# Kernel tuning notes

Measured on AMD Instinct MI355X. Metric: run time of the kernel, lower is better.

The kernel has to match this reference:

```python
import jax, jax.numpy as jnp
import numpy as np

E = 200_000   # edges (messages)
T = 2_000_000 # triplets
N = 20_000    # atoms/nodes
H = 128       # hidden_channels
INT = 64      # int_emb_size
BAS = 8       # basis_emb_size
OUT_EMB = 256 # out_emb_channels
NRAD = 6
SBF_DIM = 7 * 6  # num_spherical * num_radial = 42
NB = 4        # num_blocks
OUTC = 1      # num_targets


def setup_inputs() -> dict:
    key = jax.random.key(0)
    ks = iter(jax.random.split(key, 64))

    def w(shape):
        # glorot-ish scaled weights, stored as [in, out] for x @ W
        return jax.random.normal(next(ks), shape, jnp.float32) / np.sqrt(shape[-2])

    return dict(
        x=jax.random.normal(next(ks), (E, H), jnp.float32),
        rbf=jax.random.normal(next(ks), (E, NRAD), jnp.float32),
        sbf=jax.random.normal(next(ks), (T, SBF_DIM), jnp.float32),
        # interaction block params, stacked over NB blocks
        W_rbf1=w((NB, NRAD, BAS)), W_rbf2=w((NB, BAS, H)),
        W_sbf1=w((NB, SBF_DIM, BAS)), W_sbf2=w((NB, BAS, INT)),
        W_kj=w((NB, H, H)), b_kj=jnp.zeros((NB, H), jnp.float32),
        W_ji=w((NB, H, H)), b_ji=jnp.zeros((NB, H), jnp.float32),
        W_down=w((NB, H, INT)), W_up=w((NB, INT, H)),
        Wb=w((NB, 2, H, H)), bb=jnp.zeros((NB, 2, H), jnp.float32),   # num_before_skip=1 -> 2 linears
        Wa=w((NB, 4, H, H)), ba=jnp.zeros((NB, 4, H), jnp.float32),   # num_after_skip=2 -> 4 linears
        W_lin=w((NB, H, H)), b_lin=jnp.zeros((NB, H), jnp.float32),
        # output block params, stacked over NB+1 blocks
        Wo_rbf=w((NB + 1, NRAD, H)),
        Wo_up=w((NB + 1, H, OUT_EMB)), bo_up=jnp.zeros((NB + 1, OUT_EMB), jnp.float32),
        Wo_lins=w((NB + 1, 3, OUT_EMB, OUT_EMB)), bo_lins=jnp.zeros((NB + 1, 3, OUT_EMB), jnp.float32),
        Wo_out=w((NB + 1, OUT_EMB, OUTC)),
        idx_kj=jax.random.randint(next(ks), (T,), 0, E, jnp.int32),
        idx_ji=jax.random.randint(next(ks), (T,), 0, E, jnp.int32),
        idx_i=jax.random.randint(next(ks), (E,), 0, N, jnp.int32),
        num_nodes=N,
    )


def _interaction(b, x, rbf, sbf, idx_kj, idx_ji, p):
    act = jax.nn.silu
    x_ji = act(x @ p['W_ji'][b] + p['b_ji'][b])
    x_kj = act(x @ p['W_kj'][b] + p['b_kj'][b])
    rbf_t = (rbf @ p['W_rbf1'][b]) @ p['W_rbf2'][b]          # [E,H]
    x_kj = act((x_kj * rbf_t) @ p['W_down'][b])              # [E,INT]
    sbf_t = (sbf @ p['W_sbf1'][b]) @ p['W_sbf2'][b]          # [T,INT]
    m = x_kj[idx_kj] * sbf_t                                  # triplet gather [T,INT]
    agg = jax.ops.segment_sum(m, idx_ji, num_segments=x.shape[0])  # scatter-add [E,INT]
    x_kj = act(agg @ p['W_up'][b])                            # [E,H]
    h = x_ji + x_kj
    # residual layers before skip (1 layer = 2 linears)
    h = h + act(act(h @ p['Wb'][b, 0] + p['bb'][b, 0]) @ p['Wb'][b, 1] + p['bb'][b, 1])
    h = act(h @ p['W_lin'][b] + p['b_lin'][b]) + x
    # residual layers after skip (2 layers = 4 linears)
    for l in range(2):
        h = h + act(act(h @ p['Wa'][b, 2 * l] + p['ba'][b, 2 * l]) @ p['Wa'][b, 2 * l + 1] + p['ba'][b, 2 * l + 1])
    return h


def _output(b, x, rbf, idx_i, num_nodes, p):
    act = jax.nn.silu
    t = (rbf @ p['Wo_rbf'][b]) * x                            # [E,H]
    t = jax.ops.segment_sum(t, idx_i, num_segments=num_nodes) # [N,H]
    t = t @ p['Wo_up'][b] + p['bo_up'][b]
    for l in range(3):
        t = act(t @ p['Wo_lins'][b, l] + p['bo_lins'][b, l])
    return t @ p['Wo_out'][b]                                 # [N,OUTC]


def reference(x, rbf, sbf, W_rbf1, W_rbf2, W_sbf1, W_sbf2, W_kj, b_kj, W_ji, b_ji,
              W_down, W_up, Wb, bb, Wa, ba, W_lin, b_lin,
              Wo_rbf, Wo_up, bo_up, Wo_lins, bo_lins, Wo_out,
              idx_kj, idx_ji, idx_i, num_nodes):
    p = dict(W_rbf1=W_rbf1, W_rbf2=W_rbf2, W_sbf1=W_sbf1, W_sbf2=W_sbf2,
             W_kj=W_kj, b_kj=b_kj, W_ji=W_ji, b_ji=b_ji, W_down=W_down, W_up=W_up,
             Wb=Wb, bb=bb, Wa=Wa, ba=ba, W_lin=W_lin, b_lin=b_lin,
             Wo_rbf=Wo_rbf, Wo_up=Wo_up, bo_up=bo_up,
             Wo_lins=Wo_lins, bo_lins=bo_lins, Wo_out=Wo_out)
    P = _output(0, x, rbf, idx_i, num_nodes, p)
    for b in range(NB):  # fixed small layer loop
        x = _interaction(b, x, rbf, sbf, idx_kj, idx_ji, p)
        P = P + _output(b + 1, x, rbf, idx_i, num_nodes, p)
    return P
```

## Files before the change

kernel.cpp:

```cpp
#include <hip/hip_runtime.h>
#include <hip/hip_bf16.h>

#define E_EDGES 200000
#define T_TRIP  2000000
#define N_NODES 20000
#define H_DIM   128
#define INT_DIM 64
#define BAS     8
#define OUT_EMB 256
#define NRAD    6
#define SBF_D   42
#define NB      4

typedef __attribute__((ext_vector_type(8))) __bf16 bf16x8;
typedef __attribute__((ext_vector_type(4))) float f32x4;
typedef unsigned short u16;

__device__ __forceinline__ float silu_f(float v) { return v / (1.0f + __expf(-v)); }

__device__ __forceinline__ u16 f2bf(float f) {
    unsigned int u = __float_as_uint(f);
    u += 0x7FFF + ((u >> 16) & 1);
    return (u16)(u >> 16);
}
__device__ __forceinline__ float bf2f(u16 h) {
    return __uint_as_float(((unsigned int)h) << 16);
}

__device__ __forceinline__ void st_split4(char* H, char* L, int row, int col0, int stride,
                                          const float v[4]) {
    ushort4 hh, ll;
    u16 h0 = f2bf(v[0]); ll.x = f2bf(v[0] - bf2f(h0)); hh.x = h0;
    u16 h1 = f2bf(v[1]); ll.y = f2bf(v[1] - bf2f(h1)); hh.y = h1;
    u16 h2 = f2bf(v[2]); ll.z = f2bf(v[2] - bf2f(h2)); hh.z = h2;
    u16 h3 = f2bf(v[3]); ll.w = f2bf(v[3] - bf2f(h3)); hh.w = h3;
    int off = (row * stride + col0 * 2) ^ ((row & 7) << 4);
    *reinterpret_cast<ushort4*>(H + off) = hh;
    *reinterpret_cast<ushort4*>(L + off) = ll;
}
__device__ __forceinline__ void ld_split4(const char* H, const char* L, int row, int col0,
                                          int stride, float v[4]) {
    int off = (row * stride + col0 * 2) ^ ((row & 7) << 4);
    ushort4 hh = *reinterpret_cast<const ushort4*>(H + off);
    ushort4 ll = *reinterpret_cast<const ushort4*>(L + off);
    v[0] = bf2f(hh.x) + bf2f(ll.x);
    v[1] = bf2f(hh.y) + bf2f(ll.y);
    v[2] = bf2f(hh.z) + bf2f(ll.z);
    v[3] = bf2f(hh.w) + bf2f(ll.w);
}
__device__ __forceinline__ void st_bf4(char* T, int row, int col0, int stride,
                                       const float v[4]) {
    ushort4 hh;
    hh.x = f2bf(v[0]); hh.y = f2bf(v[1]); hh.z = f2bf(v[2]); hh.w = f2bf(v[3]);
    int off = (row * stride + col0 * 2) ^ ((row & 7) << 4);
    *reinterpret_cast<ushort4*>(T + off) = hh;
}

struct BF8x4 { bf16x8 h[4]; bf16x8 l[4]; };

__device__ __forceinline__ BF8x4 loadB128f(const u16* __restrict__ Bh, const u16* __restrict__ Bl,
                                           int k0, int wn, int l15, int khalf)
{
    BF8x4 f;
    #pragma unroll
    for (int n = 0; n < 4; ++n) {
        size_t bo = (size_t)(wn * 64 + n * 16 + l15) * 128 + k0 + khalf;
        f.h[n] = *reinterpret_cast<const bf16x8*>(Bh + bo);
        f.l[n] = *reinterpret_cast<const bf16x8*>(Bl + bo);
    }
    return f;
}
__device__ __forceinline__ BF8x4 loadB64f(const u16* __restrict__ Bh, const u16* __restrict__ Bl,
                                          int k0, int wn, int l15, int khalf)
{
    BF8x4 f;
    #pragma unroll
    for (int n = 0; n < 4; ++n) {
        size_t bo = (size_t)(wn * 64 + n * 16 + l15) * 64 + k0 + khalf;
        f.h[n] = *reinterpret_cast<const bf16x8*>(Bh + bo);
        f.l[n] = *reinterpret_cast<const bf16x8*>(Bl + bo);
    }
    return f;
}
__device__ __forceinline__ BF8x4 loadB256f(const u16* __restrict__ Bh, const u16* __restrict__ Bl,
                                           int k0, int wn, int l15, int khalf)
{
    BF8x4 f;
    #pragma unroll
    for (int n = 0; n < 4; ++n) {
        size_t bo = (size_t)(wn * 64 + n * 16 + l15) * 256 + k0 + khalf;
        f.h[n] = *reinterpret_cast<const bf16x8*>(Bh + bo);
        f.l[n] = *reinterpret_cast<const bf16x8*>(Bl + bo);
    }
    return f;
}

__device__ __forceinline__ void mfma_cluster(
    const char* AH, const char* AL, int k0, int wm, int l15, int khalf,
    const BF8x4& b, f32x4 acc[2][4])
{
    __builtin_amdgcn_s_setprio(1);
    #pragma unroll
    for (int m = 0; m < 2; ++m) {
        int row = wm * 32 + m * 16 + l15;
        int off = (row * 256 + (k0 + khalf) * 2) ^ ((row & 7) << 4);
        bf16x8 ah = *reinterpret_cast<const bf16x8*>(AH + off);
        bf16x8 al = *reinterpret_cast<const bf16x8*>(AL + off);
        #pragma unroll
        for (int n = 0; n < 4; ++n) {
            acc[m][n] = __builtin_amdgcn_mfma_f32_16x16x32_bf16(b.h[n], ah, acc[m][n], 0, 0, 0);
            acc[m][n] = __builtin_amdgcn_mfma_f32_16x16x32_bf16(b.h[n], al, acc[m][n], 0, 0, 0);
            acc[m][n] = __builtin_amdgcn_mfma_f32_16x16x32_bf16(b.l[n], ah, acc[m][n], 0, 0, 0);
        }
    }
    __builtin_amdgcn_s_setprio(0);
}
__device__ __forceinline__ void mfma_cluster_T(
    const char* T, int k0, int wm, int l15, int khalf,
    const BF8x4& b, f32x4 acc[2][4])
{
    __builtin_amdgcn_s_setprio(1);
    #pragma unroll
    for (int m = 0; m < 2; ++m) {
        int row = wm * 32 + m * 16 + l15;
        int off = (row * 256 + (k0 + khalf) * 2) ^ ((row & 7) << 4);
        bf16x8 a = *reinterpret_cast<const bf16x8*>(T + off);
        #pragma unroll
        for (int n = 0; n < 4; ++n) {
            acc[m][n] = __builtin_amdgcn_mfma_f32_16x16x32_bf16(b.h[n], a, acc[m][n], 0, 0, 0);
            acc[m][n] = __builtin_amdgcn_mfma_f32_16x16x32_bf16(b.l[n], a, acc[m][n], 0, 0, 0);
        }
    }
    __builtin_amdgcn_s_setprio(0);
}
__device__ __forceinline__ void mfma_cluster64_T(
    const char* T, int k0, int wm, int l15, int khalf,
    const BF8x4& b, f32x4 acc[2][4])
{
    __builtin_amdgcn_s_setprio(1);
    #pragma unroll
    for (int m = 0; m < 2; ++m) {
        int row = wm * 32 + m * 16 + l15;
        int off = (row * 128 + (k0 + khalf) * 2) ^ ((row & 7) << 4);
        bf16x8 a = *reinterpret_cast<const bf16x8*>(T + off);
        #pragma unroll
        for (int n = 0; n < 4; ++n) {
            acc[m][n] = __builtin_amdgcn_mfma_f32_16x16x32_bf16(b.h[n], a, acc[m][n], 0, 0, 0);
            acc[m][n] = __builtin_amdgcn_mfma_f32_16x16x32_bf16(b.l[n], a, acc[m][n], 0, 0, 0);
        }
    }
    __builtin_amdgcn_s_setprio(0);
}
__device__ __forceinline__ void mfma_cluster512(
    const char* AH, const char* AL, int k0, int l15, int khalf,
    const BF8x4& b, f32x4 acc[2][4])
{
    __builtin_amdgcn_s_setprio(1);
    #pragma unroll
    for (int m = 0; m < 2; ++m) {
        int row = m * 16 + l15;
        int off = (row * 512 + (k0 + khalf) * 2) ^ ((row & 7) << 4);
        bf16x8 ah = *reinterpret_cast<const bf16x8*>(AH + off);
        bf16x8 al = *reinterpret_cast<const bf16x8*>(AL + off);
        #pragma unroll
        for (int n = 0; n < 4; ++n) {
            acc[m][n] = __builtin_amdgcn_mfma_f32_16x16x32_bf16(b.h[n], ah, acc[m][n], 0, 0, 0);
            acc[m][n] = __builtin_amdgcn_mfma_f32_16x16x32_bf16(b.h[n], al, acc[m][n], 0, 0, 0);
            acc[m][n] = __builtin_amdgcn_mfma_f32_16x16x32_bf16(b.l[n], ah, acc[m][n], 0, 0, 0);
        }
    }
    __builtin_amdgcn_s_setprio(0);
}
__device__ __forceinline__ void mfma_cluster512_T(
    const char* T, int k0, int l15, int khalf,
    const BF8x4& b, f32x4 acc[2][4])
{
    __builtin_amdgcn_s_setprio(1);
    #pragma unroll
    for (int m = 0; m < 2; ++m) {
        int row = m * 16 + l15;
        int off = (row * 512 + (k0 + khalf) * 2) ^ ((row & 7) << 4);
        bf16x8 a = *reinterpret_cast<const bf16x8*>(T + off);
        #pragma unroll
        for (int n = 0; n < 4; ++n) {
            acc[m][n] = __builtin_amdgcn_mfma_f32_16x16x32_bf16(b.h[n], a, acc[m][n], 0, 0, 0);
            acc[m][n] = __builtin_amdgcn_mfma_f32_16x16x32_bf16(b.l[n], a, acc[m][n], 0, 0, 0);
        }
    }
    __builtin_amdgcn_s_setprio(0);
}

__device__ __forceinline__ void mm128_pipe(
    const char* AH, const char* AL,
    const u16* __restrict__ Bh, const u16* __restrict__ Bl, BF8x4& pre,
    const u16* __restrict__ nBh, const u16* __restrict__ nBl,
    int wm, int wn, int l15, int khalf, f32x4 acc[2][4])
{
    BF8x4 c0 = pre;
    BF8x4 c1 = loadB128f(Bh, Bl, 32, wn, l15, khalf);
    mfma_cluster(AH, AL, 0, wm, l15, khalf, c0, acc);
    BF8x4 c2 = loadB128f(Bh, Bl, 64, wn, l15, khalf);
    mfma_cluster(AH, AL, 32, wm, l15, khalf, c1, acc);
    BF8x4 c3 = loadB128f(Bh, Bl, 96, wn, l15, khalf);
    mfma_cluster(AH, AL, 64, wm, l15, khalf, c2, acc);
    if (nBh) pre = loadB128f(nBh, nBl, 0, wn, l15, khalf);
    mfma_cluster(AH, AL, 96, wm, l15, khalf, c3, acc);
}
__device__ __forceinline__ void mm128_pipe_T(
    const char* T,
    const u16* __restrict__ Bh, const u16* __restrict__ Bl, BF8x4& pre,
    const u16* __restrict__ nBh, const u16* __restrict__ nBl,
    int wm, int wn, int l15, int khalf, f32x4 acc[2][4])
{
    BF8x4 c0 = pre;
    BF8x4 c1 = loadB128f(Bh, Bl, 32, wn, l15, khalf);
    mfma_cluster_T(T, 0, wm, l15, khalf, c0, acc);
    BF8x4 c2 = loadB128f(Bh, Bl, 64, wn, l15, khalf);
    mfma_cluster_T(T, 32, wm, l15, khalf, c1, acc);
    BF8x4 c3 = loadB128f(Bh, Bl, 96, wn, l15, khalf);
    mfma_cluster_T(T, 64, wm, l15, khalf, c2, acc);
    if (nBh) pre = loadB128f(nBh, nBl, 0, wn, l15, khalf);
    mfma_cluster_T(T, 96, wm, l15, khalf, c3, acc);
}
__device__ __forceinline__ void mm64_pipe_T(
    const char* T,
    const u16* __restrict__ Bh, const u16* __restrict__ Bl, BF8x4& pre,
    const u16* __restrict__ nBh, const u16* __restrict__ nBl,
    int wm, int wn, int l15, int khalf, f32x4 acc[2][4])
{
    BF8x4 c0 = pre;
    BF8x4 c1 = loadB64f(Bh, Bl, 32, wn, l15, khalf);
    mfma_cluster64_T(T, 0, wm, l15, khalf, c0, acc);
    if (nBh) pre = loadB128f(nBh, nBl, 0, wn, l15, khalf);
    mfma_cluster64_T(T, 32, wm, l15, khalf, c1, acc);
}

__global__ __launch_bounds__(256) void wprep(
    const float* __restrict__ src, u16* __restrict__ hi,
    u16* __restrict__ lo, int K, int N)
{
    int e = blockIdx.x * 256 + threadIdx.x;
    int total = K * N;
    if (e >= total) return;
    size_t base = (size_t)blockIdx.y * total;
    float a = src[base + e];
    int k = e / N, n = e - k * N;
    u16 h = f2bf(a);
    u16 l = f2bf(a - bf2f(h));
    hi[base + (size_t)n * K + k] = h;
    lo[base + (size_t)n * K + k] = l;
}

__global__ __launch_bounds__(256) void cvt_bf(
    const float* __restrict__ src, u16* __restrict__ dst, int n4)
{
    int i = blockIdx.x * 256 + threadIdx.x;
    if (i >= n4) return;
    float4 f = *reinterpret_cast<const float4*>(&src[(size_t)i * 4]);
    ushort4 o;
    o.x = f2bf(f.x); o.y = f2bf(f.y); o.z = f2bf(f.z); o.w = f2bf(f.w);
    *reinterpret_cast<ushort4*>(&dst[(size_t)i * 4]) = o;
}

__global__ __launch_bounds__(256, 2) void pre_fuse(
    const u16* __restrict__ X, const float* __restrict__ rbf,
    const float* __restrict__ W1,
    const u16* __restrict__ Wjih, const u16* __restrict__ Wjil, const float* __restrict__ bji,
    const u16* __restrict__ Wkjh, const u16* __restrict__ Wkjl, const float* __restrict__ bkj,
    const float* __restrict__ Wr2,
    const u16* __restrict__ Wdnh, const u16* __restrict__ Wdnl,
    u16* __restrict__ E1, u16* __restrict__ C1)
{
    __shared__ char smem[32768];
    char* XT = smem;
    char* IT = smem + 16384;

    const int tid  = threadIdx.x;
    const int lane = tid & 63;
    const int w    = tid >> 6;
    const int wm   = w >> 1, wn = w & 1;
    const int bm   = blockIdx.x * 64;
    const int l15  = lane & 15;
    const int khalf = (lane >> 4) * 8;
    const int r4   = (lane >> 4) * 4;

    BF8x4 pre = loadB128f(Wjih, Wjil, 0, wn, l15, khalf);

    {
        int r  = tid >> 2;
        int c0 = (tid & 3) * 32;
        const u16* p = &X[(size_t)(bm + r) * H_DIM + c0];
        const int swz = (r & 7) << 4;
        #pragma unroll
        for (int q = 0; q < 4; ++q) {
            uint4 v = *reinterpret_cast<const uint4*>(p + q * 8);
            int off = (r * 256 + c0 * 2 + q * 16) ^ swz;
            *reinterpret_cast<uint4*>(XT + off) = v;
        }
    }
    __syncthreads();

    {
        f32x4 acc[2][4] = {};
        mm128_pipe_T(XT, Wjih, Wjil, pre, Wkjh, Wkjl, wm, wn, l15, khalf, acc);
        #pragma unroll
        for (int n = 0; n < 4; ++n) {
            int col0 = wn * 64 + n * 16 + r4;
            float4 bv = *reinterpret_cast<const float4*>(&bji[col0]);
            #pragma unroll
            for (int m = 0; m < 2; ++m) {
                int row = wm * 32 + m * 16 + l15;
                ushort4 ob;
                ob.x = f2bf(silu_f(acc[m][n][0] + bv.x));
                ob.y = f2bf(silu_f(acc[m][n][1] + bv.y));
                ob.z = f2bf(silu_f(acc[m][n][2] + bv.z));
                ob.w = f2bf(silu_f(acc[m][n][3] + bv.w));
                *reinterpret_cast<ushort4*>(&E1[(size_t)(bm + row) * H_DIM + col0]) = ob;
            }
        }
    }
    {
        f32x4 acc[2][4] = {};
        mm128_pipe_T(XT, Wkjh, Wkjl, pre, nullptr, nullptr, wm, wn, l15, khalf, acc);
        float r8v[2][8];
        #pragma unroll
        for (int m = 0; m < 2; ++m) {
            int grow = bm + wm * 32 + m * 16 + l15;
            const float2* rp = reinterpret_cast<const float2*>(&rbf[(size_t)grow * NRAD]);
            float2 q0 = rp[0], q1 = rp[1], q2 = rp[2];
            float rv[NRAD] = {q0.x, q0.y, q1.x, q1.y, q2.x, q2.y};
            #pragma unroll
            for (int j = 0; j < 8; ++j) r8v[m][j] = 0.f;
            #pragma unroll
            for (int k = 0; k < NRAD; ++k)
                #pragma unroll
                for (int j = 0; j < 8; ++j)
                    r8v[m][j] = fmaf(rv[k], W1[k * BAS + j], r8v[m][j]);
        }
        #pragma unroll
        for (int n = 0; n < 4; ++n) {
            int col0 = wn * 64 + n * 16 + r4;
            float4 bvf = *reinterpret_cast<const float4*>(&bkj[col0]);
            float bv[4] = {bvf.x, bvf.y, bvf.z, bvf.w};
            float wrv[8][4];
            #pragma unroll
            for (int j = 0; j < 8; ++j) {
                float4 wf = *reinterpret_cast<const float4*>(&Wr2[j * H_DIM + col0]);
                wrv[j][0] = wf.x; wrv[j][1] = wf.y; wrv[j][2] = wf.z; wrv[j][3] = wf.w;
            }
            #pragma unroll
            for (int m = 0; m < 2; ++m) {
                int row = wm * 32 + m * 16 + l15;
                float v[4];
                #pragma unroll
                for (int r = 0; r < 4; ++r) {
                    float t = silu_f(acc[m][n][r] + bv[r]);
                    float g = 0.f;
                    #pragma unroll
                    for (int j = 0; j < 8; ++j)
                        g = fmaf(r8v[m][j], wrv[j][r], g);
                    v[r] = t * g;
                }
                st_bf4(IT, row, col0, 256, v);
            }
        }
    }
    __syncthreads();

    {
        f32x4 acc[2][2] = {};
        #pragma unroll
        for (int k0 = 0; k0 < 128; k0 += 32) {
            bf16x8 bh[2], bl[2];
            #pragma unroll
            for (int n = 0; n < 2; ++n) {
                size_t bo = (size_t)(wn * 32 + n * 16 + l15) * 128 + k0 + khalf;
                bh[n] = *reinterpret_cast<const bf16x8*>(Wdnh + bo);
                bl[n] = *reinterpret_cast<const bf16x8*>(Wdnl + bo);
            }
            __builtin_amdgcn_s_setprio(1);
            #pragma unroll
            for (int m = 0; m < 2; ++m) {
                int row = wm * 32 + m * 16 + l15;
                int off = (row * 256 + (k0 + khalf) * 2) ^ ((row & 7) << 4);
                bf16x8 a = *reinterpret_cast<const bf16x8*>(IT + off);
                #pragma unroll
                for (int n = 0; n < 2; ++n) {
                    acc[m][n] = __builtin_amdgcn_mfma_f32_16x16x32_bf16(bh[n], a, acc[m][n], 0, 0, 0);
                    acc[m][n] = __builtin_amdgcn_mfma_f32_16x16x32_bf16(bl[n], a, acc[m][n], 0, 0, 0);
                }
            }
            __builtin_amdgcn_s_setprio(0);
        }
        #pragma unroll
        for (int n = 0; n < 2; ++n) {
            int col0 = wn * 32 + n * 16 + r4;
            #pragma unroll
            for (int m = 0; m < 2; ++m) {
                int row = wm * 32 + m * 16 + l15;
                ushort4 ob;
                ob.x = f2bf(silu_f(acc[m][n][0]));
                ob.y = f2bf(silu_f(acc[m][n][1]));
                ob.z = f2bf(silu_f(acc[m][n][2]));
                ob.w = f2bf(silu_f(acc[m][n][3]));
                *reinterpret_cast<ushort4*>(&C1[(size_t)(bm + row) * INT_DIM + col0]) = ob;
            }
        }
    }
}

struct ChainP {
    const u16 *uph, *upl;
    const u16 *b0h, *b0l, *b1h, *b1l;
    const u16 *lnh, *lnl;
    const u16 *a0h, *a0l, *a1h, *a1l, *a2h, *a2l, *a3h, *a3l;
    const float *bb0, *bb1, *blin, *ba0, *ba1, *ba2, *ba3;
    int doPre;
    const float *rbfp, *preW1, *nbji, *nbkj, *nwr2;
    const u16 *njih, *njil, *nkjh, *nkjl, *ndnh, *ndnl;
    u16 *nE1, *nC1;
};
struct OutP {
    const float* TN;
    const u16 *Uh, *Ul; const float* bu;
    const u16 *L0h, *L0l; const float* b0;
    const u16 *L1h, *L1l; const float* b1;
    const u16 *L2h, *L2l; const float* b2;
    const float* Wo; float* P;
};

__device__ __forceinline__ void post_chain_body(
    char* smem, int bx,
    const u16* __restrict__ AGG, const u16* __restrict__ E1,
    const u16* __restrict__ X, const ChainP& p, u16* __restrict__ OUT)
{
    char* SH  = smem;
    char* SL  = smem + 16384;
    char* TMP = smem + 32768;
    char* GB  = TMP;

    const int tid  = threadIdx.x;
    const int lane = tid & 63;
    const int w    = tid >> 6;
    const int wm   = w >> 1, wn = w & 1;
    const int bm   = bx * 64;
    const int l15  = lane & 15;
    const int khalf = (lane >> 4) * 8;
    const int r4   = (lane >> 4) * 4;

    BF8x4 pre = loadB64f(p.uph, p.upl, 0, wn, l15, khalf);

    {
        int r  = tid >> 2;
        int c0 = (tid & 3) * 16;
        const ushort4* pg = reinterpret_cast<const ushort4*>(&AGG[(size_t)(bm + r) * INT_DIM + c0]);
        const int swz = (r & 7) << 4;
        #pragma unroll
        for (int q = 0; q < 4; ++q) {
            ushort4 v = pg[q];
            int off = (r * 128 + c0 * 2 + q * 8) ^ swz;
            *reinterpret_cast<ushort4*>(GB + off) = v;
        }
    }
    __syncthreads();

    f32x4 acc[2][4];
    #define ZACC { _Pragma("unroll") for (int m = 0; m < 2; ++m) \
                   _Pragma("unroll") for (int n = 0; n < 4; ++n) \
                       acc[m][n] = f32x4{0.f, 0.f, 0.f, 0.f}; }

    ZACC
    mm64_pipe_T(GB, p.uph, p.upl, pre, p.b0h, p.b0l, wm, wn, l15, khalf, acc);
    #pragma unroll
    for (int n = 0; n < 4; ++n) {
        int col0 = wn * 64 + n * 16 + r4;
        #pragma unroll
        for (int m = 0; m < 2; ++m) {
            int row = wm * 32 + m * 16 + l15;
            ushort4 e = *reinterpret_cast<const ushort4*>(&E1[(size_t)(bm + row) * H_DIM + col0]);
            float v[4];
            v[0] = bf2f(e.x) + silu_f(acc[m][n][0]);
            v[1] = bf2f(e.y) + silu_f(acc[m][n][1]);
            v[2] = bf2f(e.z) + silu_f(acc[m][n][2]);
            v[3] = bf2f(e.w) + silu_f(acc[m][n][3]);
            st_split4(SH, SL, row, col0, 256, v);
        }
    }
    __syncthreads();

    #define STAGE_PLAIN(WH, WL, BIAS, NWH, NWL)                                         \
    {                                                                                   \
        ZACC                                                                            \
        mm128_pipe(SH, SL, WH, WL, pre, NWH, NWL, wm, wn, l15, khalf, acc);             \
        _Pragma("unroll")                                                               \
        for (int n = 0; n < 4; ++n) {                                                   \
            int col0 = wn * 64 + n * 16 + r4;                                           \
            float4 bv = *reinterpret_cast<const float4*>(&BIAS[col0]);                  \
            _Pragma("unroll")                                                           \
            for (int m = 0; m < 2; ++m) {                                               \
                int row = wm * 32 + m * 16 + l15;                                       \
                float v[4];                                                             \
                v[0] = silu_f(acc[m][n][0] + bv.x);                                     \
                v[1] = silu_f(acc[m][n][1] + bv.y);                                     \
                v[2] = silu_f(acc[m][n][2] + bv.z);                                     \
                v[3] = silu_f(acc[m][n][3] + bv.w);                                     \
                st_bf4(TMP, row, col0, 256, v);                                         \
            }                                                                           \
        }                                                                               \
        __syncthreads();                                                                \
    }

    #define STAGE_RES(WH, WL, BIAS, NWH, NWL)                                           \
    {                                                                                   \
        ZACC                                                                            \
        mm128_pipe_T(TMP, WH, WL, pre, NWH, NWL, wm, wn, l15, khalf, acc);              \
        _Pragma("unroll")                                                               \
        for (int n = 0; n < 4; ++n) {                                                   \
            int col0 = wn * 64 + n * 16 + r4;                                           \
            float4 bv = *reinterpret_cast<const float4*>(&BIAS[col0]);                  \
            _Pragma("unroll")                                                           \
            for (int m = 0; m < 2; ++m) {                                               \
                int row = wm * 32 + m * 16 + l15;                                       \
                float v[4];                                                             \
                ld_split4(SH, SL, row, col0, 256, v);                                   \
                v[0] += silu_f(acc[m][n][0] + bv.x);                                    \
                v[1] += silu_f(acc[m][n][1] + bv.y);                                    \
                v[2] += silu_f(acc[m][n][2] + bv.z);                                    \
                v[3] += silu_f(acc[m][n][3] + bv.w);                                    \
                st_split4(SH, SL, row, col0, 256, v);                                   \
            }                                                                           \
        }                                                                               \
        __syncthreads();                                                                \
    }

    STAGE_PLAIN(p.b0h, p.b0l, p.bb0, p.b1h, p.b1l)
    STAGE_RES(p.b1h, p.b1l, p.bb1, p.lnh, p.lnl)

    {
        ZACC
        mm128_pipe(SH, SL, p.lnh, p.lnl, pre, p.a0h, p.a0l, wm, wn, l15, khalf, acc);
        __syncthreads();
        #pragma unroll
        for (int n = 0; n < 4; ++n) {
            int col0 = wn * 64 + n * 16 + r4;
            float4 bv = *reinterpret_cast<const float4*>(&p.blin[col0]);
            #pragma unroll
            for (int m = 0; m < 2; ++m) {
                int row = wm * 32 + m * 16 + l15;
                ushort4 xv = *reinterpret_cast<const ushort4*>(&X[(size_t)(bm + row) * H_DIM + col0]);
                float v[4];
                v[0] = silu_f(acc[m][n][0] + bv.x) + bf2f(xv.x);
                v[1] = silu_f(acc[m][n][1] + bv.y) + bf2f(xv.y);
                v[2] = silu_f(acc[m][n][2] + bv.z) + bf2f(xv.z);
                v[3] = silu_f(acc[m][n][3] + bv.w) + bf2f(xv.w);
                st_split4(SH, SL, row, col0, 256, v);
            }
        }
        __syncthreads();
    }

    STAGE_PLAIN(p.a0h, p.a0l, p.ba0, p.a1h, p.a1l)
    STAGE_RES(p.a1h, p.a1l, p.ba1, p.a2h, p.a2l)
    STAGE_PLAIN(p.a2h, p.a2l, p.ba2, p.a3h, p.a3l)

    {
        ZACC
        mm128_pipe_T(TMP, p.a3h, p.a3l, pre,
                     p.doPre ? p.njih : nullptr, p.doPre ? p.njil : nullptr,
                     wm, wn, l15, khalf, acc);
        #pragma unroll
        for (int n = 0; n < 4; ++n) {
            int col0 = wn * 64 + n * 16 + r4;
            float4 bv = *reinterpret_cast<const float4*>(&p.ba3[col0]);
            #pragma unroll
            for (int m = 0; m < 2; ++m) {
                int row = wm * 32 + m * 16 + l15;
                float v[4];
                ld_split4(SH, SL, row, col0, 256, v);
                ushort4 ob;
                ob.x = f2bf(v[0] + silu_f(acc[m][n][0] + bv.x));
                ob.y = f2bf(v[1] + silu_f(acc[m][n][1] + bv.y));
                ob.z = f2bf(v[2] + silu_f(acc[m][n][2] + bv.z));
                ob.w = f2bf(v[3] + silu_f(acc[m][n][3] + bv.w));
                *reinterpret_cast<ushort4*>(&OUT[(size_t)(bm + row) * H_DIM + col0]) = ob;
                if (p.doPre) {
                    int offx = (row * 256 + col0 * 2) ^ ((row & 7) << 4);
                    *reinterpret_cast<ushort4*>(SH + offx) = ob;
                }
            }
        }
    }

    if (p.doPre) {
        char* XT = SH;
        char* IT = SL;
        __syncthreads();

        {
            ZACC
            mm128_pipe_T(XT, p.njih, p.njil, pre, p.nkjh, p.nkjl, wm, wn, l15, khalf, acc);
            #pragma unroll
            for (int n = 0; n < 4; ++n) {
                int col0 = wn * 64 + n * 16 + r4;
                float4 bv = *reinterpret_cast<const float4*>(&p.nbji[col0]);
                #pragma unroll
                for (int m = 0; m < 2; ++m) {
                    int row = wm * 32 + m * 16 + l15;
                    ushort4 ob;
                    ob.x = f2bf(silu_f(acc[m][n][0] + bv.x));
                    ob.y = f2bf(silu_f(acc[m][n][1] + bv.y));
                    ob.z = f2bf(silu_f(acc[m][n][2] + bv.z));
                    ob.w = f2bf(silu_f(acc[m][n][3] + bv.w));
                    *reinterpret_cast<ushort4*>(&p.nE1[(size_t)(bm + row) * H_DIM + col0]) = ob;
                }
            }
        }
        {
            ZACC
            mm128_pipe_T(XT, p.nkjh, p.nkjl, pre, nullptr, nullptr, wm, wn, l15, khalf, acc);
            float r8v[2][8];
            #pragma unroll
            for (int m = 0; m < 2; ++m) {
                int grow = bm + wm * 32 + m * 16 + l15;
                const float2* rp = reinterpret_cast<const float2*>(&p.rbfp[(size_t)grow * NRAD]);
                float2 q0 = rp[0], q1 = rp[1], q2 = rp[2];
                float rv[NRAD] = {q0.x, q0.y, q1.x, q1.y, q2.x, q2.y};
                #pragma unroll
                for (int j = 0; j < 8; ++j) r8v[m][j] = 0.f;
                #pragma unroll
                for (int k = 0; k < NRAD; ++k)
                    #pragma unroll
                    for (int j = 0; j < 8; ++j)
                        r8v[m][j] = fmaf(rv[k], p.preW1[k * BAS + j], r8v[m][j]);
            }
            #pragma unroll
            for (int n = 0; n < 4; ++n) {
                int col0 = wn * 64 + n * 16 + r4;
                float4 bvf = *reinterpret_cast<const float4*>(&p.nbkj[col0]);
                float bv[4] = {bvf.x, bvf.y, bvf.z, bvf.w};
                float wrv[8][4];
                #pragma unroll
                for (int j = 0; j < 8; ++j) {
                    float4 wf = *reinterpret_cast<const float4*>(&p.nwr2[j * H_DIM + col0]);
                    wrv[j][0] = wf.x; wrv[j][1] = wf.y; wrv[j][2] = wf.z; wrv[j][3] = wf.w;
                }
                #pragma unroll
                for (int m = 0; m < 2; ++m) {
                    int row = wm * 32 + m * 16 + l15;
                    float v[4];
                    #pragma unroll
                    for (int r = 0; r < 4; ++r) {
                        float t = silu_f(acc[m][n][r] + bv[r]);
                        float g = 0.f;
                        #pragma unroll
                        for (int j = 0; j < 8; ++j)
                            g = fmaf(r8v[m][j], wrv[j][r], g);
                        v[r] = t * g;
                    }
                    st_bf4(IT, row, col0, 256, v);
                }
            }
        }
        __syncthreads();

        {
            f32x4 acc2[2][2] = {};
            #pragma unroll
            for (int k0 = 0; k0 < 128; k0 += 32) {
                bf16x8 bh[2], bl[2];
                #pragma unroll
                for (int n = 0; n < 2; ++n) {
                    size_t bo = (size_t)(wn * 32 + n * 16 + l15) * 128 + k0 + khalf;
                    bh[n] = *reinterpret_cast<const bf16x8*>(p.ndnh + bo);
                    bl[n] = *reinterpret_cast<const bf16x8*>(p.ndnl + bo);
                }
                __builtin_amdgcn_s_setprio(1);
                #pragma unroll
                for (int m = 0; m < 2; ++m) {
                    int row = wm * 32 + m * 16 + l15;
                    int off = (row * 256 + (k0 + khalf) * 2) ^ ((row & 7) << 4);
                    bf16x8 a = *reinterpret_cast<const bf16x8*>(IT + off);
                    #pragma unroll
                    for (int n = 0; n < 2; ++n) {
                        acc2[m][n] = __builtin_amdgcn_mfma_f32_16x16x32_bf16(bh[n], a, acc2[m][n], 0, 0, 0);
                        acc2[m][n] = __builtin_amdgcn_mfma_f32_16x16x32_bf16(bl[n], a, acc2[m][n], 0, 0, 0);
                    }
                }
                __builtin_amdgcn_s_setprio(0);
            }
            #pragma unroll
            for (int n = 0; n < 2; ++n) {
                int col0 = wn * 32 + n * 16 + r4;
                #pragma unroll
                for (int m = 0; m < 2; ++m) {
                    int row = wm * 32 + m * 16 + l15;
                    ushort4 ob;
                    ob.x = f2bf(silu_f(acc2[m][n][0]));
                    ob.y = f2bf(silu_f(acc2[m][n][1]));
                    ob.z = f2bf(silu_f(acc2[m][n][2]));
                    ob.w = f2bf(silu_f(acc2[m][n][3]));
                    *reinterpret_cast<ushort4*>(&p.nC1[(size_t)(bm + row) * INT_DIM + col0]) = ob;
                }
            }
        }
    }
    #undef STAGE_PLAIN
    #undef STAGE_RES
    #undef ZACC
}

__device__ __forceinline__ void out_chain_body(char* smem, int bx, const OutP& o)
{
    char* SH  = smem;
    char* SL  = smem + 16384;
    char* TMP = smem + 32768;
    char* XH  = TMP;
    char* XL  = TMP + 8192;

    const int tid  = threadIdx.x;
    const int lane = tid & 63;
    const int wn   = tid >> 6;
    const int bm   = bx * 32;
    const int l15  = lane & 15;
    const int khalf = (lane >> 4) * 8;
    const int r4   = (lane >> 4) * 4;

    {
        int r  = tid >> 3;
        int c0 = (tid & 7) * 16;
        const float* p = &o.TN[(size_t)(bm + r) * H_DIM + c0];
        const int swz = (r & 7) << 4;
        #pragma unroll
        for (int q = 0; q < 4; ++q) {
            float4 f = *reinterpret_cast<const float4*>(p + q * 4);
            float vv[4] = {f.x, f.y, f.z, f.w};
            u16 h[4], l[4];
            #pragma unroll
            for (int j = 0; j < 4; ++j) {
                h[j] = f2bf(vv[j]);
                l[j] = f2bf(vv[j] - bf2f(h[j]));
            }
            int off = (r * 256 + c0 * 2 + q * 8) ^ swz;
            *reinterpret_cast<ushort4*>(XH + off) = make_ushort4(h[0], h[1], h[2], h[3]);
            *reinterpret_cast<ushort4*>(XL + off) = make_ushort4(l[0], l[1], l[2], l[3]);
        }
    }
    __syncthreads();

    f32x4 acc[2][4];
    #define ZACC { _Pragma("unroll") for (int m = 0; m < 2; ++m) \
                   _Pragma("unroll") for (int n = 0; n < 4; ++n) \
                       acc[m][n] = f32x4{0.f, 0.f, 0.f, 0.f}; }

    {
        ZACC
        BF8x4 cur = loadB128f(o.Uh, o.Ul, 0, wn, l15, khalf);
        #pragma unroll
        for (int k = 0; k < 4; ++k) {
            BF8x4 nxt;
            if (k < 3) nxt = loadB128f(o.Uh, o.Ul, 32 * (k + 1), wn, l15, khalf);
            mfma_cluster(XH, XL, 32 * k, 0, l15, khalf, cur, acc);
            if (k < 3) cur = nxt;
        }
        __syncthreads();
        #pragma unroll
        for (int n = 0; n < 4; ++n) {
            int col0 = wn * 64 + n * 16 + r4;
            float4 bv = *reinterpret_cast<const float4*>(&o.bu[col0]);
            #pragma unroll
            for (int m = 0; m < 2; ++m) {
                int row = m * 16 + l15;
                float v[4] = {acc[m][n][0] + bv.x, acc[m][n][1] + bv.y,
                              acc[m][n][2] + bv.z, acc[m][n][3] + bv.w};
                st_split4(SH, SL, row, col0, 512, v);
            }
        }
        __syncthreads();
    }

    {
        ZACC
        BF8x4 cur = loadB256f(o.L0h, o.L0l, 0, wn, l15, khalf);
        #pragma unroll
        for (int k = 0; k < 8; ++k) {
            BF8x4 nxt;
            if (k < 7) nxt = loadB256f(o.L0h, o.L0l, 32 * (k + 1), wn, l15, khalf);
            mfma_cluster512(SH, SL, 32 * k, l15, khalf, cur, acc);
            if (k < 7) cur = nxt;
        }
        #pragma unroll
        for (int n = 0; n < 4; ++n) {
            int col0 = wn * 64 + n * 16 + r4;
            float4 bv = *reinterpret_cast<const float4*>(&o.b0[col0]);
            #pragma unroll
            for (int m = 0; m < 2; ++m) {
                int row = m * 16 + l15;
                float v[4];
                v[0] = silu_f(acc[m][n][0] + bv.x);
                v[1] = silu_f(acc[m][n][1] + bv.y);
                v[2] = silu_f(acc[m][n][2] + bv.z);
                v[3] = silu_f(acc[m][n][3] + bv.w);
                st_bf4(TMP, row, col0, 512, v);
            }
        }
        __syncthreads();
    }

    {
        ZACC
        BF8x4 cur = loadB256f(o.L1h, o.L1l, 0, wn, l15, khalf);
        #pragma unroll
        for (int k = 0; k < 8; ++k) {
            BF8x4 nxt;
            if (k < 7) nxt = loadB256f(o.L1h, o.L1l, 32 * (k + 1), wn, l15, khalf);
            mfma_cluster512_T(TMP, 32 * k, l15, khalf, cur, acc);
            if (k < 7) cur = nxt;
        }
        #pragma unroll
        for (int n = 0; n < 4; ++n) {
            int col0 = wn * 64 + n * 16 + r4;
            float4 bv = *reinterpret_cast<const float4*>(&o.b1[col0]);
            #pragma unroll
            for (int m = 0; m < 2; ++m) {
                int row = m * 16 + l15;
                float v[4];
                v[0] = silu_f(acc[m][n][0] + bv.x);
                v[1] = silu_f(acc[m][n][1] + bv.y);
                v[2] = silu_f(acc[m][n][2] + bv.z);
                v[3] = silu_f(acc[m][n][3] + bv.w);
                st_split4(SH, SL, row, col0, 512, v);
            }
        }
        __syncthreads();
    }

    {
        ZACC
        BF8x4 cur = loadB256f(o.L2h, o.L2l, 0, wn, l15, khalf);
        #pragma unroll
        for (int k = 0; k < 8; ++k) {
            BF8x4 nxt;
            if (k < 7) nxt = loadB256f(o.L2h, o.L2l, 32 * (k + 1), wn, l15, khalf);
            mfma_cluster512(SH, SL, 32 * k, l15, khalf, cur, acc);
            if (k < 7) cur = nxt;
        }
        __syncthreads();
        #pragma unroll
        for (int n = 0; n < 4; ++n) {
            int col0 = wn * 64 + n * 16 + r4;
            float4 bv = *reinterpret_cast<const float4*>(&o.b2[col0]);
            #pragma unroll
            for (int m = 0; m < 2; ++m) {
                int row = m * 16 + l15;
                float v[4];
                v[0] = silu_f(acc[m][n][0] + bv.x);
                v[1] = silu_f(acc[m][n][1] + bv.y);
                v[2] = silu_f(acc[m][n][2] + bv.z);
                v[3] = silu_f(acc[m][n][3] + bv.w);
                st_split4(SH, SL, row, col0, 512, v);
            }
        }
        __syncthreads();
    }

    {
        int row  = tid >> 3;
        int part = tid & 7;
        float s = 0.f;
        int cbase = part * 32;
        #pragma unroll
        for (int c4 = 0; c4 < 32; c4 += 4) {
            float v[4];
            ld_split4(SH, SL, row, cbase + c4, 512, v);
            float4 wv = *reinterpret_cast<const float4*>(&o.Wo[cbase + c4]);
            s = fmaf(v[0], wv.x, s);
            s = fmaf(v[1], wv.y, s);
            s = fmaf(v[2], wv.z, s);
            s = fmaf(v[3], wv.w, s);
        }
        s += __shfl_xor(s, 1);
        s += __shfl_xor(s, 2);
        s += __shfl_xor(s, 4);
        if (part == 0) o.P[bm + row] += s;
    }
    #undef ZACC
}

__global__ __launch_bounds__(256, 2) void post_fused(
    int npost,
    const u16* __restrict__ AGG, const u16* __restrict__ E1,
    const u16* __restrict__ X, ChainP p, u16* __restrict__ OUT, OutP o)
{
    __shared__ char smem[49152];
    if ((int)blockIdx.x < npost)
        post_chain_body(smem, blockIdx.x, AGG, E1, X, p, OUT);
    else
        out_chain_body(smem, blockIdx.x - npost, o);
}

__device__ __forceinline__ float dot8_bf(uint4 r, const float* w2) {
    float s;
    s  = bf2f((u16)(r.x)) * w2[0] + bf2f((u16)(r.x >> 16)) * w2[1];
    s += bf2f((u16)(r.y)) * w2[2] + bf2f((u16)(r.y >> 16)) * w2[3];
    s += bf2f((u16)(r.z)) * w2[4] + bf2f((u16)(r.z >> 16)) * w2[5];
    s += bf2f((u16)(r.w)) * w2[6] + bf2f((u16)(r.w >> 16)) * w2[7];
    return s;
}

__device__ __forceinline__ void triplet_body(
    int bx, int nblk,
    const u16* __restrict__ ps8b, const float* __restrict__ Wsb2,
    const u16* __restrict__ xkj, const int* __restrict__ pkj,
    const int* __restrict__ tptr, const int* __restrict__ tcnt,
    u16* __restrict__ agg)
{
    const int lane = threadIdx.x & 63;
    int wid = bx * 4 + (threadIdx.x >> 6);
    const int nw = nblk * 4;
    float w2[BAS];
    #pragma unroll
    for (int j = 0; j < BAS; ++j) w2[j] = Wsb2[j * INT_DIM + lane];

    for (int e = wid; e < E_EDGES; e += nw) {
        int start = tptr[e];
        int end   = start + tcnt[e];
        float acc0 = 0.f, acc1 = 0.f;
        int i = start;
        for (; i + 1 < end; i += 2) {
            uint4 ra = *reinterpret_cast<const uint4*>(&ps8b[(size_t)i * BAS]);
            uint4 rb = *reinterpret_cast<const uint4*>(&ps8b[(size_t)(i + 1) * BAS]);
            int e0 = pkj[i], e1 = pkj[i + 1];
            float s0 = dot8_bf(ra, w2);
            float s1 = dot8_bf(rb, w2);
            acc0 = fmaf(bf2f(xkj[(size_t)e0 * INT_DIM + lane]), s0, acc0);
            acc1 = fmaf(bf2f(xkj[(size_t)e1 * INT_DIM + lane]), s1, acc1);
        }
        if (i < end) {
            uint4 ra = *reinterpret_cast<const uint4*>(&ps8b[(size_t)i * BAS]);
            int e0 = pkj[i];
            acc0 = fmaf(bf2f(xkj[(size_t)e0 * INT_DIM + lane]), dot8_bf(ra, w2), acc0);
        }
        agg[(size_t)e * INT_DIM + lane] = f2bf(acc0 + acc1);
    }
}

__device__ __forceinline__ void out_gather_body(
    int bx, int nblk,
    const float* __restrict__ rbf, const float* __restrict__ Wor,
    const u16* __restrict__ x,
    const int* __restrict__ eptr, const int* __restrict__ ecnt,
    const int* __restrict__ eperm, float* __restrict__ tN)
{
    const int lane = threadIdx.x & 63;
    int wid = bx * 4 + (threadIdx.x >> 6);
    const int nw = nblk * 4;
    float wr0[NRAD], wr1[NRAD];
    #pragma unroll
    for (int k = 0; k < NRAD; ++k) {
        wr0[k] = Wor[k * H_DIM + lane];
        wr1[k] = Wor[k * H_DIM + lane + 64];
    }
    for (int n = wid; n < N_NODES; n += nw) {
        int start = eptr[n];
        int end   = start + ecnt[n];
        float a0 = 0.f, a1 = 0.f;
        for (int i = start; i < end; ++i) {
            int e = eperm[i];
            const float2* rp = reinterpret_cast<const float2*>(&rbf[(size_t)e * NRAD]);
            float2 r0 = rp[0], r1 = rp[1], r2 = rp[2];
            float rA = r0.x*wr0[0] + r0.y*wr0[1] + r1.x*wr0[2]
                     + r1.y*wr0[3] + r2.x*wr0[4] + r2.y*wr0[5];
            float rB = r0.x*wr1[0] + r0.y*wr1[1] + r1.x*wr1[2]
                     + r1.y*wr1[3] + r2.x*wr1[4] + r2.y*wr1[5];
            a0 = fmaf(rA, bf2f(x[(size_t)e * H_DIM + lane]), a0);
            a1 = fmaf(rB, bf2f(x[(size_t)e * H_DIM + lane + 64]), a1);
        }
        tN[(size_t)n * H_DIM + lane] = a0;
        tN[(size_t)n * H_DIM + lane + 64] = a1;
    }
}

__global__ __launch_bounds__(256) void gather_fused(
    int GT,
    const u16* __restrict__ ps8b, const float* __restrict__ Wsb2,
    const u16* __restrict__ xkj, const int* __restrict__ pkj,
    const int* __restrict__ tptr, const int* __restrict__ tcnt,
    u16* __restrict__ agg,
    const float* __restrict__ rbf, const float* __restrict__ Wor,
    const u16* __restrict__ x,
    const int* __restrict__ eptr, const int* __restrict__ ecnt,
    const int* __restrict__ eperm, float* __restrict__ tN)
{
    int bx = blockIdx.x;
    if (bx < GT)
        triplet_body(bx, GT, ps8b, Wsb2, xkj, pkj, tptr, tcnt, agg);
    else
        out_gather_body(bx - GT, gridDim.x - GT, rbf, Wor, x, eptr, ecnt, eperm, tN);
}

__global__ __launch_bounds__(256) void csr_count(
    const int* __restrict__ idx, int* __restrict__ cnt, int n)
{
    int i = blockIdx.x * 256 + threadIdx.x;
    if (i < n) atomicAdd(&cnt[idx[i]], 1);
}

__global__ __launch_bounds__(256) void scan_block(
    const int* __restrict__ cnt, int* __restrict__ ptr, int* __restrict__ bsum, int n)
{
    __shared__ int s[256];
    int i = blockIdx.x * 256 + threadIdx.x;
    int v = (i < n) ? cnt[i] : 0;
    s[threadIdx.x] = v;
    __syncthreads();
    #pragma unroll
    for (int off = 1; off < 256; off <<= 1) {
        int t = (threadIdx.x >= off) ? s[threadIdx.x - off] : 0;
        __syncthreads();
        s[threadIdx.x] += t;
        __syncthreads();
    }
    if (i < n) ptr[i] = s[threadIdx.x] - v;
    if (threadIdx.x == 255) bsum[blockIdx.x] = s[255];
}

__global__ __launch_bounds__(1024) void scan_aux(int* __restrict__ bsum, int nb)
{
    __shared__ int s[1024];
    int v = (threadIdx.x < nb) ? bsum[threadIdx.x] : 0;
    s[threadIdx.x] = v;
    __syncthreads();
    #pragma unroll
    for (int off = 1; off < 1024; off <<= 1) {
        int t = (threadIdx.x >= off) ? s[threadIdx.x - off] : 0;
        __syncthreads();
        s[threadIdx.x] += t;
        __syncthreads();
    }
    if (threadIdx.x < nb) bsum[threadIdx.x] = s[threadIdx.x] - v;
}

__global__ __launch_bounds__(256) void scan_add(
    int* __restrict__ ptr, const int* __restrict__ bsum, int n)
{
    int i = blockIdx.x * 256 + threadIdx.x;
    if (i < n) ptr[i] += bsum[blockIdx.x];
// ... 258 lines not shown
```

Baseline: 3.878 ms.

## Drop split-bf16 activations in post/output chains, shrink LDS and raise occupancy

Activations held in shared memory for the post-interaction and output-block chains were stored as hi+lo bf16 pairs and multiplied with three MFMAs per tile. They are now stored as a single bf16 value and use the two-MFMA path, with the weights still split. This halves the LDS footprint from 48KB to 32KB, so launch bounds are raised to 4 blocks per CU, and it removes a third of the MFMA work plus the split conversions. The cost is lower precision for intermediate activations and for the residual stream kept in shared memory, which could push outputs past the tolerance.

```diff
diff --git a/kernel.cpp b/kernel.cpp
--- a/kernel.cpp
+++ b/kernel.cpp
@@ -27,27 +27,6 @@
     return __uint_as_float(((unsigned int)h) << 16);
 }
 
-__device__ __forceinline__ void st_split4(char* H, char* L, int row, int col0, int stride,
-                                          const float v[4]) {
-    ushort4 hh, ll;
-    u16 h0 = f2bf(v[0]); ll.x = f2bf(v[0] - bf2f(h0)); hh.x = h0;
-    u16 h1 = f2bf(v[1]); ll.y = f2bf(v[1] - bf2f(h1)); hh.y = h1;
-    u16 h2 = f2bf(v[2]); ll.z = f2bf(v[2] - bf2f(h2)); hh.z = h2;
-    u16 h3 = f2bf(v[3]); ll.w = f2bf(v[3] - bf2f(h3)); hh.w = h3;
-    int off = (row * stride + col0 * 2) ^ ((row & 7) << 4);
-    *reinterpret_cast<ushort4*>(H + off) = hh;
-    *reinterpret_cast<ushort4*>(L + off) = ll;
-}
-__device__ __forceinline__ void ld_split4(const char* H, const char* L, int row, int col0,
-                                          int stride, float v[4]) {
-    int off = (row * stride + col0 * 2) ^ ((row & 7) << 4);
-    ushort4 hh = *reinterpret_cast<const ushort4*>(H + off);
-    ushort4 ll = *reinterpret_cast<const ushort4*>(L + off);
-    v[0] = bf2f(hh.x) + bf2f(ll.x);
-    v[1] = bf2f(hh.y) + bf2f(ll.y);
-    v[2] = bf2f(hh.z) + bf2f(ll.z);
-    v[3] = bf2f(hh.w) + bf2f(ll.w);
-}
 __device__ __forceinline__ void st_bf4(char* T, int row, int col0, int stride,
                                        const float v[4]) {
     ushort4 hh;
@@ -55,6 +34,12 @@
     int off = (row * stride + col0 * 2) ^ ((row & 7) << 4);
     *reinterpret_cast<ushort4*>(T + off) = hh;
 }
+__device__ __forceinline__ void ld_bf4(const char* T, int row, int col0, int stride,
+                                       float v[4]) {
+    int off = (row * stride + col0 * 2) ^ ((row & 7) << 4);
+    ushort4 hh = *reinterpret_cast<const ushort4*>(T + off);
+    v[0] = bf2f(hh.x); v[1] = bf2f(hh.y); v[2] = bf2f(hh.z); v[3] = bf2f(hh.w);
+}
 
 struct BF8x4 { bf16x8 h[4]; bf16x8 l[4]; };
 
@@ -95,26 +80,6 @@
     return f;
 }
 
-__device__ __forceinline__ void mfma_cluster(
-    const char* AH, const char* AL, int k0, int wm, int l15, int khalf,
-    const BF8x4& b, f32x4 acc[2][4])
-{
-    __builtin_amdgcn_s_setprio(1);
-    #pragma unroll
-    for (int m = 0; m < 2; ++m) {
-        int row = wm * 32 + m * 16 + l15;
-        int off = (row * 256 + (k0 + khalf) * 2) ^ ((row & 7) << 4);
-        bf16x8 ah = *reinterpret_cast<const bf16x8*>(AH + off);
-        bf16x8 al = *reinterpret_cast<const bf16x8*>(AL + off);
-        #pragma unroll
-        for (int n = 0; n < 4; ++n) {
-            acc[m][n] = __builtin_amdgcn_mfma_f32_16x16x32_bf16(b.h[n], ah, acc[m][n], 0, 0, 0);
-            acc[m][n] = __builtin_amdgcn_mfma_f32_16x16x32_bf16(b.h[n], al, acc[m][n], 0, 0, 0);
-            acc[m][n] = __builtin_amdgcn_mfma_f32_16x16x32_bf16(b.l[n], ah, acc[m][n], 0, 0, 0);
-        }
-    }
-    __builtin_amdgcn_s_setprio(0);
-}
 __device__ __forceinline__ void mfma_cluster_T(
     const char* T, int k0, int wm, int l15, int khalf,
     const BF8x4& b, f32x4 acc[2][4])
@@ -151,26 +116,6 @@
     }
     __builtin_amdgcn_s_setprio(0);
 }
-__device__ __forceinline__ void mfma_cluster512(
-    const char* AH, const char* AL, int k0, int l15, int khalf,
-    const BF8x4& b, f32x4 acc[2][4])
-{
-    __builtin_amdgcn_s_setprio(1);
-    #pragma unroll
-    for (int m = 0; m < 2; ++m) {
-        int row = m * 16 + l15;
-        int off = (row * 512 + (k0 + khalf) * 2) ^ ((row & 7) << 4);
-        bf16x8 ah = *reinterpret_cast<const bf16x8*>(AH + off);
-        bf16x8 al = *reinterpret_cast<const bf16x8*>(AL + off);
-        #pragma unroll
-        for (int n = 0; n < 4; ++n) {
-            acc[m][n] = __builtin_amdgcn_mfma_f32_16x16x32_bf16(b.h[n], ah, acc[m][n], 0, 0, 0);
-            acc[m][n] = __builtin_amdgcn_mfma_f32_16x16x32_bf16(b.h[n], al, acc[m][n], 0, 0, 0);
-            acc[m][n] = __builtin_amdgcn_mfma_f32_16x16x32_bf16(b.l[n], ah, acc[m][n], 0, 0, 0);
-        }
-    }
-    __builtin_amdgcn_s_setprio(0);
-}
 __device__ __forceinline__ void mfma_cluster512_T(
     const char* T, int k0, int l15, int khalf,
     const BF8x4& b, f32x4 acc[2][4])
@@ -190,22 +135,6 @@
     __builtin_amdgcn_s_setprio(0);
 }
 
-__device__ __forceinline__ void mm128_pipe(
-    const char* AH, const char* AL,
-    const u16* __restrict__ Bh, const u16* __restrict__ Bl, BF8x4& pre,
-    const u16* __restrict__ nBh, const u16* __restrict__ nBl,
-    int wm, int wn, int l15, int khalf, f32x4 acc[2][4])
-{
-    BF8x4 c0 = pre;
-    BF8x4 c1 = loadB128f(Bh, Bl, 32, wn, l15, khalf);
-    mfma_cluster(AH, AL, 0, wm, l15, khalf, c0, acc);
-    BF8x4 c2 = loadB128f(Bh, Bl, 64, wn, l15, khalf);
-    mfma_cluster(AH, AL, 32, wm, l15, khalf, c1, acc);
-    BF8x4 c3 = loadB128f(Bh, Bl, 96, wn, l15, khalf);
-    mfma_cluster(AH, AL, 64, wm, l15, khalf, c2, acc);
-    if (nBh) pre = loadB128f(nBh, nBl, 0, wn, l15, khalf);
-    mfma_cluster(AH, AL, 96, wm, l15, khalf, c3, acc);
-}
 __device__ __forceinline__ void mm128_pipe_T(
     const char* T,
     const u16* __restrict__ Bh, const u16* __restrict__ Bl, BF8x4& pre,
@@ -434,10 +363,9 @@
     const u16* __restrict__ AGG, const u16* __restrict__ E1,
     const u16* __restrict__ X, const ChainP& p, u16* __restrict__ OUT)
 {
-    char* SH  = smem;
-    char* SL  = smem + 16384;
-    char* TMP = smem + 32768;
-    char* GB  = TMP;
+    char* SB = smem;
+    char* TB = smem + 16384;
+    char* GB = TB;
 
     const int tid  = threadIdx.x;
     const int lane = tid & 63;
@@ -483,7 +411,7 @@
             v[1] = bf2f(e.y) + silu_f(acc[m][n][1]);
             v[2] = bf2f(e.z) + silu_f(acc[m][n][2]);
             v[3] = bf2f(e.w) + silu_f(acc[m][n][3]);
-            st_split4(SH, SL, row, col0, 256, v);
+            st_bf4(SB, row, col0, 256, v);
         }
     }
     __syncthreads();
@@ -491,7 +419,7 @@
     #define STAGE_PLAIN(WH, WL, BIAS, NWH, NWL)                                         \
     {                                                                                   \
         ZACC                                                                            \
-        mm128_pipe(SH, SL, WH, WL, pre, NWH, NWL, wm, wn, l15, khalf, acc);             \
+        mm128_pipe_T(SB, WH, WL, pre, NWH, NWL, wm, wn, l15, khalf, acc);               \
         _Pragma("unroll")                                                               \
         for (int n = 0; n < 4; ++n) {                                                   \
             int col0 = wn * 64 + n * 16 + r4;                                           \
@@ -504,7 +432,7 @@
                 v[1] = silu_f(acc[m][n][1] + bv.y);                                     \
                 v[2] = silu_f(acc[m][n][2] + bv.z);                                     \
                 v[3] = silu_f(acc[m][n][3] + bv.w);                                     \
-                st_bf4(TMP, row, col0, 256, v);                                         \
+                st_bf4(TB, row, col0, 256, v);                                          \
             }                                                                           \
         }                                                                               \
         __syncthreads();                                                                \
@@ -513,7 +441,7 @@
     #define STAGE_RES(WH, WL, BIAS, NWH, NWL)                                           \
     {                                                                                   \
         ZACC                                                                            \
-        mm128_pipe_T(TMP, WH, WL, pre, NWH, NWL, wm, wn, l15, khalf, acc);              \
+        mm128_pipe_T(TB, WH, WL, pre, NWH, NWL, wm, wn, l15, khalf, acc);               \
         _Pragma("unroll")                                                               \
         for (int n = 0; n < 4; ++n) {                                                   \
             int col0 = wn * 64 + n * 16 + r4;                                           \
@@ -522,12 +450,12 @@
             for (int m = 0; m < 2; ++m) {                                               \
                 int row = wm * 32 + m * 16 + l15;                                       \
                 float v[4];                                                             \
-                ld_split4(SH, SL, row, col0, 256, v);                                   \
+                ld_bf4(SB, row, col0, 256, v);                                          \
                 v[0] += silu_f(acc[m][n][0] + bv.x);                                    \
                 v[1] += silu_f(acc[m][n][1] + bv.y);                                    \
                 v[2] += silu_f(acc[m][n][2] + bv.z);                                    \
                 v[3] += silu_f(acc[m][n][3] + bv.w);                                    \
-                st_split4(SH, SL, row, col0, 256, v);                                   \
+                st_bf4(SB, row, col0, 256, v);                                          \
             }                                                                           \
         }                                                                               \
         __syncthreads();                                                                \
@@ -538,7 +466,7 @@
 
     {
         ZACC
-        mm128_pipe(SH, SL, p.lnh, p.lnl, pre, p.a0h, p.a0l, wm, wn, l15, khalf, acc);
+        mm128_pipe_T(SB, p.lnh, p.lnl, pre, p.a0h, p.a0l, wm, wn, l15, khalf, acc);
         __syncthreads();
         #pragma unroll
         for (int n = 0; n < 4; ++n) {
@@ -553,7 +481,7 @@
                 v[1] = silu_f(acc[m][n][1] + bv.y) + bf2f(xv.y);
                 v[2] = silu_f(acc[m][n][2] + bv.z) + bf2f(xv.z);
                 v[3] = silu_f(acc[m][n][3] + bv.w) + bf2f(xv.w);
-                st_split4(SH, SL, row, col0, 256, v);
+                st_bf4(SB, row, col0, 256, v);
             }
         }
         __syncthreads();
@@ -565,7 +493,7 @@
 
     {
         ZACC
-        mm128_pipe_T(TMP, p.a3h, p.a3l, pre,
+        mm128_pipe_T(TB, p.a3h, p.a3l, pre,
                      p.doPre ? p.njih : nullptr, p.doPre ? p.njil : nullptr,
                      wm, wn, l15, khalf, acc);
         #pragma unroll
@@ -576,7 +504,7 @@
             for (int m = 0; m < 2; ++m) {
                 int row = wm * 32 + m * 16 + l15;
                 float v[4];
-                ld_split4(SH, SL, row, col0, 256, v);
+                ld_bf4(SB, row, col0, 256, v);
                 ushort4 ob;
                 ob.x = f2bf(v[0] + silu_f(acc[m][n][0] + bv.x));
                 ob.y = f2bf(v[1] + silu_f(acc[m][n][1] + bv.y));
@@ -585,15 +513,15 @@
                 *reinterpret_cast<ushort4*>(&OUT[(size_t)(bm + row) * H_DIM + col0]) = ob;
                 if (p.doPre) {
                     int offx = (row * 256 + col0 * 2) ^ ((row & 7) << 4);
-                    *reinterpret_cast<ushort4*>(SH + offx) = ob;
+                    *reinterpret_cast<ushort4*>(SB + offx) = ob;
                 }
             }
         }
     }
 
     if (p.doPre) {
-        char* XT = SH;
-        char* IT = SL;
+        char* XT = SB;
+        char* IT = TB;
         __syncthreads();
 
         {
@@ -711,11 +639,8 @@
 
 __device__ __forceinline__ void out_chain_body(char* smem, int bx, const OutP& o)
 {
-    char* SH  = smem;
-    char* SL  = smem + 16384;
-    char* TMP = smem + 32768;
-    char* XH  = TMP;
-    char* XL  = TMP + 8192;
+    char* RA = smem;
+    char* RB = smem + 16384;
 
     const int tid  = threadIdx.x;
     const int lane = tid & 63;
@@ -733,16 +658,10 @@
         #pragma unroll
         for (int q = 0; q < 4; ++q) {
             float4 f = *reinterpret_cast<const float4*>(p + q * 4);
-            float vv[4] = {f.x, f.y, f.z, f.w};
-            u16 h[4], l[4];
-            #pragma unroll
-            for (int j = 0; j < 4; ++j) {
-                h[j] = f2bf(vv[j]);
-                l[j] = f2bf(vv[j] - bf2f(h[j]));
-            }
+            ushort4 hh;
+            hh.x = f2bf(f.x); hh.y = f2bf(f.y); hh.z = f2bf(f.z); hh.w = f2bf(f.w);
             int off = (r * 256 + c0 * 2 + q * 8) ^ swz;
-            *reinterpret_cast<ushort4*>(XH + off) = make_ushort4(h[0], h[1], h[2], h[3]);
-            *reinterpret_cast<ushort4*>(XL + off) = make_ushort4(l[0], l[1], l[2], l[3]);
+            *reinterpret_cast<ushort4*>(RA + off) = hh;
         }
     }
     __syncthreads();
@@ -754,15 +673,8 @@
 
     {
         ZACC
-        BF8x4 cur = loadB128f(o.Uh, o.Ul, 0, wn, l15, khalf);
-        #pragma unroll
-        for (int k = 0; k < 4; ++k) {
-            BF8x4 nxt;
-            if (k < 3) nxt = loadB128f(o.Uh, o.Ul, 32 * (k + 1), wn, l15, khalf);
-            mfma_cluster(XH, XL, 32 * k, 0, l15, khalf, cur, acc);
-            if (k < 3) cur = nxt;
-        }
-        __syncthreads();
+        BF8x4 pre = loadB128f(o.Uh, o.Ul, 0, wn, l15, khalf);
+        mm128_pipe_T(RA, o.Uh, o.Ul, pre, nullptr, nullptr, 0, wn, l15, khalf, acc);
         #pragma unroll
         for (int n = 0; n < 4; ++n) {
             int col0 = wn * 64 + n * 16 + r4;
@@ -772,7 +684,7 @@
                 int row = m * 16 + l15;
                 float v[4] = {acc[m][n][0] + bv.x, acc[m][n][1] + bv.y,
                               acc[m][n][2] + bv.z, acc[m][n][3] + bv.w};
-                st_split4(SH, SL, row, col0, 512, v);
+                st_bf4(RB, row, col0, 512, v);
             }
         }
         __syncthreads();
@@ -785,7 +697,7 @@
         for (int k = 0; k < 8; ++k) {
             BF8x4 nxt;
             if (k < 7) nxt = loadB256f(o.L0h, o.L0l, 32 * (k + 1), wn, l15, khalf);
-            mfma_cluster512(SH, SL, 32 * k, l15, khalf, cur, acc);
+            mfma_cluster512_T(RB, 32 * k, l15, khalf, cur, acc);
             if (k < 7) cur = nxt;
         }
         #pragma unroll
@@ -800,7 +712,7 @@
                 v[1] = silu_f(acc[m][n][1] + bv.y);
                 v[2] = silu_f(acc[m][n][2] + bv.z);
                 v[3] = silu_f(acc[m][n][3] + bv.w);
-                st_bf4(TMP, row, col0, 512, v);
+                st_bf4(RA, row, col0, 512, v);
             }
         }
         __syncthreads();
@@ -813,7 +725,7 @@
         for (int k = 0; k < 8; ++k) {
             BF8x4 nxt;
             if (k < 7) nxt = loadB256f(o.L1h, o.L1l, 32 * (k + 1), wn, l15, khalf);
-            mfma_cluster512_T(TMP, 32 * k, l15, khalf, cur, acc);
+            mfma_cluster512_T(RA, 32 * k, l15, khalf, cur, acc);
             if (k < 7) cur = nxt;
         }
         #pragma unroll
@@ -828,7 +740,7 @@
                 v[1] = silu_f(acc[m][n][1] + bv.y);
                 v[2] = silu_f(acc[m][n][2] + bv.z);
                 v[3] = silu_f(acc[m][n][3] + bv.w);
-                st_split4(SH, SL, row, col0, 512, v);
+                st_bf4(RB, row, col0, 512, v);
             }
         }
         __syncthreads();
@@ -841,7 +753,7 @@
         for (int k = 0; k < 8; ++k) {
             BF8x4 nxt;
             if (k < 7) nxt = loadB256f(o.L2h, o.L2l, 32 * (k + 1), wn, l15, khalf);
-            mfma_cluster512(SH, SL, 32 * k, l15, khalf, cur, acc);
+            mfma_cluster512_T(RB, 32 * k, l15, khalf, cur, acc);
             if (k < 7) cur = nxt;
         }
         __syncthreads();
@@ -857,7 +769,7 @@
                 v[1] = silu_f(acc[m][n][1] + bv.y);
                 v[2] = silu_f(acc[m][n][2] + bv.z);
                 v[3] = silu_f(acc[m][n][3] + bv.w);
-                st_split4(SH, SL, row, col0, 512, v);
+                st_bf4(RB, row, col0, 512, v);
             }
         }
         __syncthreads();
@@ -871,7 +783,7 @@
         #pragma unroll
         for (int c4 = 0; c4 < 32; c4 += 4) {
             float v[4];
-            ld_split4(SH, SL, row, cbase + c4, 512, v);
+            ld_bf4(RB, row, cbase + c4, 512, v);
             float4 wv = *reinterpret_cast<const float4*>(&o.Wo[cbase + c4]);
             s = fmaf(v[0], wv.x, s);
             s = fmaf(v[1], wv.y, s);
@@ -886,12 +798,12 @@
     #undef ZACC
 }
 
-__global__ __launch_bounds__(256, 2) void post_fused(
+__global__ __launch_bounds__(256, 4) void post_fused(
     int npost,
     const u16* __restrict__ AGG, const u16* __restrict__ E1,
     const u16* __restrict__ X, ChainP p, u16* __restrict__ OUT, OutP o)
 {
-    __shared__ char smem[49152];
+    __shared__ char smem[32768];
     if ((int)blockIdx.x < npost)
         post_chain_body(smem, blockIdx.x, AGG, E1, X, p, OUT);
     else
```

Result: slower. 4.840 ms (+24.8%).
